# Optimization experiments

Hardware: AMD Instinct MI355X
Metric: run time of the kernel (lower is better)

The kernel has to match this reference:

```python
import jax, jax.numpy as jnp
import numpy as np

NEG_SLOPE = 0.2
LN_EPS = 1e-5


def setup_inputs() -> dict:
    key = jax.random.key(0)
    kx, kw, ks, kd = jax.random.split(key, 4)
    B, T, C, Fin, Fout = 32, 256, 64, 128, 128
    x = jax.random.normal(kx, (B, T, C, Fin), dtype=jnp.float32)
    W = jax.random.normal(kw, (Fin, Fout), dtype=jnp.float32) * (1.0 / np.sqrt(Fin))
    attn_src = jax.random.normal(ks, (Fout,), dtype=jnp.float32) * 0.1
    attn_dst = jax.random.normal(kd, (Fout,), dtype=jnp.float32) * 0.1
    gamma = jnp.ones((Fout,), dtype=jnp.float32)
    beta = jnp.zeros((Fout,), dtype=jnp.float32)
    return {"x": x, "W": W, "attn_src": attn_src, "attn_dst": attn_dst,
            "gamma": gamma, "beta": beta}


def reference(x, W, attn_src, attn_dst, gamma, beta):
    # h: (B,T,C,Fout)
    h = jnp.einsum('btci,io->btco', x, W)
    src = jnp.einsum('btcf,f->btc', h, attn_src)  # score of node as source
    dst = jnp.einsum('btcf,f->btc', h, attn_dst)  # score of node as dest
    # e[b,t,i,j] = src[b,t,i] + dst[b,t,j]
    e = src[..., :, None] + dst[..., None, :]
    e = jnp.where(e >= 0, e, NEG_SLOPE * e)  # leaky_relu
    alpha = jax.nn.softmax(e, axis=-1)       # softmax over neighbors j
    out = jnp.einsum('btij,btjf->btif', alpha, h)
    # LayerNorm over feature dim
    mu = jnp.mean(out, axis=-1, keepdims=True)
    var = jnp.var(out, axis=-1, keepdims=True)
    out = (out - mu) * jax.lax.rsqrt(var + LN_EPS) * gamma + beta
    return jax.nn.relu(out)
```

## Files before the change

### kernel.cpp

```cpp
#include <hip/hip_runtime.h>


typedef __attribute__((ext_vector_type(8))) short short8;
typedef __attribute__((ext_vector_type(4))) float f32x4;

constexpr int   NTILES    = 8192;
constexpr int   GRID      = 768;
constexpr float NEG_SLOPE = 0.2f;
constexpr float LN_EPS    = 1e-5f;

__device__ __forceinline__ unsigned short f2bf(float f) {
    unsigned int u = __builtin_bit_cast(unsigned int, f);
    return (unsigned short)((u + 0x7FFFu + ((u >> 16) & 1u)) >> 16);
}
__device__ __forceinline__ unsigned pack2(float lo, float hi) {
    return (unsigned)f2bf(lo) | ((unsigned)f2bf(hi) << 16);
}
__device__ __forceinline__ unsigned swz256(int row, int bytecol) {
    return (unsigned)(row * 256 + bytecol) ^ (unsigned)((row & 7) << 4);
}
__device__ __forceinline__ unsigned swz128(int row, int bytecol) {
    return (unsigned)(row * 128 + bytecol) ^ (unsigned)((row & 7) << 4);
}

#define LBAR() do { asm volatile("s_waitcnt lgkmcnt(0)"); __builtin_amdgcn_s_barrier(); } while (0)

__launch_bounds__(256, 3)
__global__ void gat_mfma7(const float* __restrict__ x,
                          const float* __restrict__ W,
                          const float* __restrict__ a_src,
                          const float* __restrict__ a_dst,
                          const float* __restrict__ gamma,
                          const float* __restrict__ beta,
                          float* __restrict__ out)
{
    __shared__ __align__(16) unsigned short sWt[128 * 128];
    __shared__ __align__(16) unsigned short sXH[64 * 128];
    __shared__ __align__(16) float s_src[64];
    __shared__ __align__(16) float s_dst[64];
    __shared__ __align__(16) float s_ws[128];
    __shared__ __align__(16) float s_wd[128];
    __shared__ __align__(16) float s_g[128];
    __shared__ __align__(16) float s_b[128];

    const int t    = threadIdx.x;
    const int lane = t & 63;
    const int w    = t >> 6;
    const int l15  = lane & 15;
    const int lg   = lane >> 4;

    if (t < 128) {
        const float4* W4  = reinterpret_cast<const float4*>(W) + t * 32;
        const float4* as4 = reinterpret_cast<const float4*>(a_src);
        const float4* ad4 = reinterpret_cast<const float4*>(a_dst);
        float ws = 0.f, wd = 0.f;
        for (int n4 = 0; n4 < 32; ++n4) {
            float4 wr = W4[n4], as = as4[n4], ad = ad4[n4];
            ws += wr.x*as.x + wr.y*as.y + wr.z*as.z + wr.w*as.w;
            wd += wr.x*ad.x + wr.y*ad.y + wr.z*ad.z + wr.w*ad.w;
        }
        s_ws[t] = ws; s_wd[t] = wd;
        s_g[t] = gamma[t]; s_b[t] = beta[t];
    }

    {
        const float4* W4 = reinterpret_cast<const float4*>(W);
        for (int c = 0; c < 16; ++c) {
            int idx4 = t + 256 * c;
            float4 v = W4[idx4];
            int k  = idx4 >> 5;
            int n0 = (idx4 & 31) << 2;
            *(unsigned short*)((char*)sWt + swz256(n0 + 0, k * 2)) = f2bf(v.x);
            *(unsigned short*)((char*)sWt + swz256(n0 + 1, k * 2)) = f2bf(v.y);
            *(unsigned short*)((char*)sWt + swz256(n0 + 2, k * 2)) = f2bf(v.z);
            *(unsigned short*)((char*)sWt + swz256(n0 + 3, k * 2)) = f2bf(v.w);
        }
    }
    __syncthreads();

    float wsr[8], wdr[8];
    {
        const int k0 = (t & 15) * 8;
        #pragma unroll
        for (int q = 0; q < 8; ++q) { wsr[q] = s_ws[k0 + q]; wdr[q] = s_wd[k0 + q]; }
    }

    float4 px[8];
    {
        const float4* x4 = reinterpret_cast<const float4*>(x + (size_t)blockIdx.x * 8192);
        #pragma unroll
        for (int c = 0; c < 4; ++c) {
            const int idx8 = t + 256 * c;
            px[2*c]   = x4[idx8 * 2];
            px[2*c+1] = x4[idx8 * 2 + 1];
        }
    }

    for (int tile = blockIdx.x; tile < NTILES; tile += GRID) {
        float* ob = out + (size_t)tile * 8192;

        #pragma unroll
        for (int c = 0; c < 4; ++c) {
            const float4 v0 = px[2*c], v1 = px[2*c+1];
            float ps = v0.x*wsr[0] + v0.y*wsr[1] + v0.z*wsr[2] + v0.w*wsr[3]
                     + v1.x*wsr[4] + v1.y*wsr[5] + v1.z*wsr[6] + v1.w*wsr[7];
            float pd = v0.x*wdr[0] + v0.y*wdr[1] + v0.z*wdr[2] + v0.w*wdr[3]
                     + v1.x*wdr[4] + v1.y*wdr[5] + v1.z*wdr[6] + v1.w*wdr[7];
            uint4 pk;
            pk.x = pack2(v0.x, v0.y); pk.y = pack2(v0.z, v0.w);
            pk.z = pack2(v1.x, v1.y); pk.w = pack2(v1.z, v1.w);
            const int m = (t >> 4) + 16 * c;
            *(uint4*)((char*)sXH + swz256(m, (t & 15) * 16)) = pk;
            #pragma unroll
            for (int msk = 1; msk < 16; msk <<= 1) {
                ps += __shfl_xor(ps, msk, 64);
                pd += __shfl_xor(pd, msk, 64);
            }
            if ((t & 15) == 0) { s_src[m] = ps; s_dst[m] = pd; }
        }

        if (tile + GRID < NTILES) {
            const float4* xn = reinterpret_cast<const float4*>(x + (size_t)(tile + GRID) * 8192);
            #pragma unroll
            for (int c = 0; c < 4; ++c) {
                const int idx8 = t + 256 * c;
                px[2*c]   = xn[idx8 * 2];
                px[2*c+1] = xn[idx8 * 2 + 1];
            }
        }
        LBAR();

        f32x4 acc[4][2];
        #pragma unroll
        for (int mi = 0; mi < 4; ++mi) {
            acc[mi][0] = f32x4{0.f,0.f,0.f,0.f};
            acc[mi][1] = f32x4{0.f,0.f,0.f,0.f};
        }
        #pragma unroll
        for (int kb = 0; kb < 4; ++kb) {
            const int kbyte = kb * 64 + lg * 16;
            short8 bfr0 = *(const short8*)((char*)sWt + swz256(32 * w +  0 + l15, kbyte));
            short8 bfr1 = *(const short8*)((char*)sWt + swz256(32 * w + 16 + l15, kbyte));
            #pragma unroll
            for (int mi = 0; mi < 4; ++mi) {
                short8 afr = *(const short8*)((char*)sXH + swz256(mi * 16 + l15, kbyte));
                acc[mi][0] = __builtin_amdgcn_mfma_f32_16x16x32_bf16(afr, bfr0, acc[mi][0], 0, 0, 0);
                acc[mi][1] = __builtin_amdgcn_mfma_f32_16x16x32_bf16(afr, bfr1, acc[mi][1], 0, 0, 0);
            }
        }

        short8 pa0, pa1;
        {
            const float srci = s_src[w * 16 + l15];
            const float4 dA0 = *(const float4*)&s_dst[lg * 8];
            const float4 dA1 = *(const float4*)&s_dst[lg * 8 + 4];
            const float4 dB0 = *(const float4*)&s_dst[32 + lg * 8];
            const float4 dB1 = *(const float4*)&s_dst[32 + lg * 8 + 4];
            float e[16] = { srci+dA0.x, srci+dA0.y, srci+dA0.z, srci+dA0.w,
                            srci+dA1.x, srci+dA1.y, srci+dA1.z, srci+dA1.w,
                            srci+dB0.x, srci+dB0.y, srci+dB0.z, srci+dB0.w,
                            srci+dB1.x, srci+dB1.y, srci+dB1.z, srci+dB1.w };
            float mx = -1e30f;
            #pragma unroll
            for (int q = 0; q < 16; ++q) {
                e[q] = (e[q] >= 0.f) ? e[q] : NEG_SLOPE * e[q];
                mx = fmaxf(mx, e[q]);
            }
            mx = fmaxf(mx, __shfl_xor(mx, 16, 64));
            mx = fmaxf(mx, __shfl_xor(mx, 32, 64));
            float sm = 0.f;
            #pragma unroll
            for (int q = 0; q < 16; ++q) { e[q] = __expf(e[q] - mx); sm += e[q]; }
            sm += __shfl_xor(sm, 16, 64);
            sm += __shfl_xor(sm, 32, 64);
            const float inv = 1.0f / sm;
            uint4 p0, p1;
            p0.x = pack2(e[0]*inv,  e[1]*inv);  p0.y = pack2(e[2]*inv,  e[3]*inv);
            p0.z = pack2(e[4]*inv,  e[5]*inv);  p0.w = pack2(e[6]*inv,  e[7]*inv);
            p1.x = pack2(e[8]*inv,  e[9]*inv);  p1.y = pack2(e[10]*inv, e[11]*inv);
            p1.z = pack2(e[12]*inv, e[13]*inv); p1.w = pack2(e[14]*inv, e[15]*inv);
            pa0 = __builtin_bit_cast(short8, p0);
            pa1 = __builtin_bit_cast(short8, p1);
        }
        LBAR();

        #pragma unroll
        for (int mi = 0; mi < 4; ++mi) {
            const int m0 = mi * 16 + lg * 4;
            #pragma unroll
            for (int nb = 0; nb < 2; ++nb) {
                const int n = 32 * w + nb * 16 + l15;
                uint2 pk;
                pk.x = pack2(acc[mi][nb][0], acc[mi][nb][1]);
                pk.y = pack2(acc[mi][nb][2], acc[mi][nb][3]);
                *(uint2*)((char*)sXH + swz128(n, m0 * 2)) = pk;
            }
        }
        LBAR();

        f32x4 o[8];
        #pragma unroll
        for (int mi = 0; mi < 8; ++mi) o[mi] = f32x4{0.f,0.f,0.f,0.f};
        #pragma unroll
        for (int kb = 0; kb < 2; ++kb) {
            const int jbyte = kb * 64 + lg * 16;
            const short8 bfr = (kb == 0) ? pa0 : pa1;
            #pragma unroll
            for (int mi = 0; mi < 8; ++mi) {
                short8 afr = *(const short8*)((char*)sXH + swz128(mi * 16 + l15, jbyte));
                o[mi] = __builtin_amdgcn_mfma_f32_16x16x32_bf16(afr, bfr, o[mi], 0, 0, 0);
            }
        }

        float sm1 = 0.f, sm2 = 0.f;
        #pragma unroll
        for (int mi = 0; mi < 8; ++mi) {
            #pragma unroll
            for (int r = 0; r < 4; ++r) { const float v = o[mi][r]; sm1 += v; sm2 += v * v; }
        }
        sm1 += __shfl_xor(sm1, 16, 64); sm2 += __shfl_xor(sm2, 16, 64);
        sm1 += __shfl_xor(sm1, 32, 64); sm2 += __shfl_xor(sm2, 32, 64);
        const float mu   = sm1 * (1.f / 128.f);
        const float var  = sm2 * (1.f / 128.f) - mu * mu;
        const float rstd = rsqrtf(var + LN_EPS);

        float* orow = ob + (w * 16 + l15) * 128;
        #pragma unroll
        for (int mi = 0; mi < 8; ++mi) {
            const int n0 = mi * 16 + lg * 4;
            const float4 gv = *(const float4*)&s_g[n0];
            const float4 bv = *(const float4*)&s_b[n0];
            float4 vo;
            vo.x = fmaxf((o[mi][0] - mu) * rstd * gv.x + bv.x, 0.f);
            vo.y = fmaxf((o[mi][1] - mu) * rstd * gv.y + bv.y, 0.f);
            vo.z = fmaxf((o[mi][2] - mu) * rstd * gv.z + bv.z, 0.f);
            vo.w = fmaxf((o[mi][3] - mu) * rstd * gv.w + bv.w, 0.f);
            *(float4*)(orow + n0) = vo;
        }
        LBAR();
    }
}

extern "C" void kernel_launch(void* const* d_in, const int* in_sizes, int n_in,
                              void* d_out, int out_size, void* d_ws, size_t ws_size,
                              hipStream_t stream) {
    const float* x   = (const float*)d_in[0];
    const float* W   = (const float*)d_in[1];
    const float* asv = (const float*)d_in[2];
    const float* adv = (const float*)d_in[3];
    const float* gm  = (const float*)d_in[4];
    const float* bt  = (const float*)d_in[5];
    float* out = (float*)d_out;

    hipLaunchKernelGGL(gat_mfma7, dim3(GRID), dim3(256), 0, stream,
                       x, W, asv, adv, gm, bt, out);
}
```

Baseline: 132.3 us.

## Double-buffer X staging and keep W fragments in registers

Moves the bf16 W operand out of shared memory into per-wave register fragments, which frees LDS for a second X/H buffer. Staging and score computation for the next tile now run one iteration ahead into the alternate buffer, and the global x prefetch goes two tiles ahead. The change removes one barrier per tile and the LDS reads of W, and adds sched_barrier fences around each barrier. In exchange it raises register pressure from 32 extra VGPRs of W fragments under a 3-blocks launch bound, and W is now read from global with strided scalar loads at startup.

Result: slower. 181.4 us (+37.1%).

```diff
diff --git a/kernel.cpp b/kernel.cpp
--- a/kernel.cpp
+++ b/kernel.cpp
@@ -23,21 +23,49 @@
     return (unsigned)(row * 128 + bytecol) ^ (unsigned)((row & 7) << 4);
 }
 
-#define LBAR() do { asm volatile("s_waitcnt lgkmcnt(0)"); __builtin_amdgcn_s_barrier(); } while (0)
+#define LBAR() do {                                              \
+    __builtin_amdgcn_sched_barrier(0);                           \
+    asm volatile("s_waitcnt lgkmcnt(0)" ::: "memory");           \
+    __builtin_amdgcn_s_barrier();                                \
+    __builtin_amdgcn_sched_barrier(0);                           \
+} while (0)
+
+#define STAGE_AND_SCORES(buf, psrc, pdst)                                     \
+    do {                                                                      \
+        _Pragma("unroll")                                                     \
+        for (int c = 0; c < 4; ++c) {                                         \
+            const float4 v0 = px[2*c], v1 = px[2*c+1];                        \
+            float ps = v0.x*wsr[0] + v0.y*wsr[1] + v0.z*wsr[2] + v0.w*wsr[3]  \
+                     + v1.x*wsr[4] + v1.y*wsr[5] + v1.z*wsr[6] + v1.w*wsr[7]; \
+            float pd = v0.x*wdr[0] + v0.y*wdr[1] + v0.z*wdr[2] + v0.w*wdr[3]  \
+                     + v1.x*wdr[4] + v1.y*wdr[5] + v1.z*wdr[6] + v1.w*wdr[7]; \
+            uint4 pk;                                                         \
+            pk.x = pack2(v0.x, v0.y); pk.y = pack2(v0.z, v0.w);               \
+            pk.z = pack2(v1.x, v1.y); pk.w = pack2(v1.z, v1.w);               \
+            const int m = (t >> 4) + 16 * c;                                  \
+            *(uint4*)((char*)(buf) + swz256(m, (t & 15) * 16)) = pk;          \
+            _Pragma("unroll")                                                 \
+            for (int msk = 1; msk < 16; msk <<= 1) {                          \
+                ps += __shfl_xor(ps, msk, 64);                                \
+                pd += __shfl_xor(pd, msk, 64);                                \
+            }                                                                 \
+            if ((t & 15) == 0) { (psrc)[m] = ps; (pdst)[m] = pd; }            \
+        }                                                                     \
+    } while (0)
 
 __launch_bounds__(256, 3)
-__global__ void gat_mfma7(const float* __restrict__ x,
-                          const float* __restrict__ W,
-                          const float* __restrict__ a_src,
-                          const float* __restrict__ a_dst,
-                          const float* __restrict__ gamma,
-                          const float* __restrict__ beta,
-                          float* __restrict__ out)
+__global__ void gat_mfma10(const float* __restrict__ x,
+                           const float* __restrict__ W,
+                           const float* __restrict__ a_src,
+                           const float* __restrict__ a_dst,
+                           const float* __restrict__ gamma,
+                           const float* __restrict__ beta,
+                           float* __restrict__ out)
 {
-    __shared__ __align__(16) unsigned short sWt[128 * 128];
-    __shared__ __align__(16) unsigned short sXH[64 * 128];
-    __shared__ __align__(16) float s_src[64];
-    __shared__ __align__(16) float s_dst[64];
+    __shared__ __align__(16) unsigned short sB0[64 * 128];
+    __shared__ __align__(16) unsigned short sB1[64 * 128];
+    __shared__ __align__(16) float s_src2[2][64];
+    __shared__ __align__(16) float s_dst2[2][64];
     __shared__ __align__(16) float s_ws[128];
     __shared__ __align__(16) float s_wd[128];
     __shared__ __align__(16) float s_g[128];
@@ -63,17 +91,20 @@
         s_g[t] = gamma[t]; s_b[t] = beta[t];
     }
 
-    {
-        const float4* W4 = reinterpret_cast<const float4*>(W);
-        for (int c = 0; c < 16; ++c) {
-            int idx4 = t + 256 * c;
-            float4 v = W4[idx4];
-            int k  = idx4 >> 5;
-            int n0 = (idx4 & 31) << 2;
-            *(unsigned short*)((char*)sWt + swz256(n0 + 0, k * 2)) = f2bf(v.x);
-            *(unsigned short*)((char*)sWt + swz256(n0 + 1, k * 2)) = f2bf(v.y);
-            *(unsigned short*)((char*)sWt + swz256(n0 + 2, k * 2)) = f2bf(v.z);
-            *(unsigned short*)((char*)sWt + swz256(n0 + 3, k * 2)) = f2bf(v.w);
+    short8 wfrag[2][4];
+    #pragma unroll
+    for (int nb = 0; nb < 2; ++nb) {
+        #pragma unroll
+        for (int kb = 0; kb < 4; ++kb) {
+            const int n = 32 * w + nb * 16 + l15;
+            float v[8];
+            #pragma unroll
+            for (int q = 0; q < 8; ++q)
+                v[q] = W[(kb * 32 + lg * 8 + q) * 128 + n];
+            uint4 pfr;
+            pfr.x = pack2(v[0], v[1]); pfr.y = pack2(v[2], v[3]);
+            pfr.z = pack2(v[4], v[5]); pfr.w = pack2(v[6], v[7]);
+            wfrag[nb][kb] = __builtin_bit_cast(short8, pfr);
         }
     }
     __syncthreads();
@@ -95,32 +126,29 @@
             px[2*c+1] = x4[idx8 * 2 + 1];
         }
     }
-
+    STAGE_AND_SCORES(sB0, s_src2[0], s_dst2[0]);
+    {
+        const float4* xn = reinterpret_cast<const float4*>(x + (size_t)(blockIdx.x + GRID) * 8192);
+        #pragma unroll
+        for (int c = 0; c < 4; ++c) {
+            const int idx8 = t + 256 * c;
+            px[2*c]   = xn[idx8 * 2];
+            px[2*c+1] = xn[idx8 * 2 + 1];
+        }
+    }
+    __syncthreads();
+
+    int p = 0;
     for (int tile = blockIdx.x; tile < NTILES; tile += GRID) {
         float* ob = out + (size_t)tile * 8192;
-
-        #pragma unroll
-        for (int c = 0; c < 4; ++c) {
-            const float4 v0 = px[2*c], v1 = px[2*c+1];
-            float ps = v0.x*wsr[0] + v0.y*wsr[1] + v0.z*wsr[2] + v0.w*wsr[3]
-                     + v1.x*wsr[4] + v1.y*wsr[5] + v1.z*wsr[6] + v1.w*wsr[7];
-            float pd = v0.x*wdr[0] + v0.y*wdr[1] + v0.z*wdr[2] + v0.w*wdr[3]
-                     + v1.x*wdr[4] + v1.y*wdr[5] + v1.z*wdr[6] + v1.w*wdr[7];
-            uint4 pk;
-            pk.x = pack2(v0.x, v0.y); pk.y = pack2(v0.z, v0.w);
-            pk.z = pack2(v1.x, v1.y); pk.w = pack2(v1.z, v1.w);
-            const int m = (t >> 4) + 16 * c;
-            *(uint4*)((char*)sXH + swz256(m, (t & 15) * 16)) = pk;
-            #pragma unroll
-            for (int msk = 1; msk < 16; msk <<= 1) {
-                ps += __shfl_xor(ps, msk, 64);
-                pd += __shfl_xor(pd, msk, 64);
-            }
-            if ((t & 15) == 0) { s_src[m] = ps; s_dst[m] = pd; }
-        }
+        unsigned short* cur = p ? sB1 : sB0;
+        unsigned short* nxt = p ? sB0 : sB1;
 
         if (tile + GRID < NTILES) {
-            const float4* xn = reinterpret_cast<const float4*>(x + (size_t)(tile + GRID) * 8192);
+            STAGE_AND_SCORES(nxt, s_src2[p ^ 1], s_dst2[p ^ 1]);
+        }
+        if (tile + 2 * GRID < NTILES) {
+            const float4* xn = reinterpret_cast<const float4*>(x + (size_t)(tile + 2 * GRID) * 8192);
             #pragma unroll
             for (int c = 0; c < 4; ++c) {
                 const int idx8 = t + 256 * c;
@@ -128,7 +156,6 @@
                 px[2*c+1] = xn[idx8 * 2 + 1];
             }
         }
-        LBAR();
 
         f32x4 acc[4][2];
         #pragma unroll
@@ -139,18 +166,33 @@
         #pragma unroll
         for (int kb = 0; kb < 4; ++kb) {
             const int kbyte = kb * 64 + lg * 16;
-            short8 bfr0 = *(const short8*)((char*)sWt + swz256(32 * w +  0 + l15, kbyte));
-            short8 bfr1 = *(const short8*)((char*)sWt + swz256(32 * w + 16 + l15, kbyte));
             #pragma unroll
             for (int mi = 0; mi < 4; ++mi) {
-                short8 afr = *(const short8*)((char*)sXH + swz256(mi * 16 + l15, kbyte));
-                acc[mi][0] = __builtin_amdgcn_mfma_f32_16x16x32_bf16(afr, bfr0, acc[mi][0], 0, 0, 0);
-                acc[mi][1] = __builtin_amdgcn_mfma_f32_16x16x32_bf16(afr, bfr1, acc[mi][1], 0, 0, 0);
-            }
-        }
+                short8 afr = *(const short8*)((char*)cur + swz256(mi * 16 + l15, kbyte));
+                acc[mi][0] = __builtin_amdgcn_mfma_f32_16x16x32_bf16(afr, wfrag[0][kb], acc[mi][0], 0, 0, 0);
+                acc[mi][1] = __builtin_amdgcn_mfma_f32_16x16x32_bf16(afr, wfrag[1][kb], acc[mi][1], 0, 0, 0);
+            }
+        }
+        LBAR();
+
+        #pragma unroll
+        for (int mi = 0; mi < 4; ++mi) {
+            const int m0 = mi * 16 + lg * 4;
+            #pragma unroll
+            for (int nb = 0; nb < 2; ++nb) {
+                const int n = 32 * w + nb * 16 + l15;
+                uint2 pk;
+                pk.x = pack2(acc[mi][nb][0], acc[mi][nb][1]);
+                pk.y = pack2(acc[mi][nb][2], acc[mi][nb][3]);
+                *(uint2*)((char*)cur + swz128(n, m0 * 2)) = pk;
+            }
+        }
+        LBAR();
 
         short8 pa0, pa1;
         {
+            const float* s_src = s_src2[p];
+            const float* s_dst = s_dst2[p];
             const float srci = s_src[w * 16 + l15];
             const float4 dA0 = *(const float4*)&s_dst[lg * 8];
             const float4 dA1 = *(const float4*)&s_dst[lg * 8 + 4];
@@ -182,21 +224,6 @@
             pa0 = __builtin_bit_cast(short8, p0);
             pa1 = __builtin_bit_cast(short8, p1);
         }
-        LBAR();
-
-        #pragma unroll
-        for (int mi = 0; mi < 4; ++mi) {
-            const int m0 = mi * 16 + lg * 4;
-            #pragma unroll
-            for (int nb = 0; nb < 2; ++nb) {
-                const int n = 32 * w + nb * 16 + l15;
-                uint2 pk;
-                pk.x = pack2(acc[mi][nb][0], acc[mi][nb][1]);
-                pk.y = pack2(acc[mi][nb][2], acc[mi][nb][3]);
-                *(uint2*)((char*)sXH + swz128(n, m0 * 2)) = pk;
-            }
-        }
-        LBAR();
 
         f32x4 o[8];
         #pragma unroll
@@ -207,7 +234,7 @@
             const short8 bfr = (kb == 0) ? pa0 : pa1;
             #pragma unroll
             for (int mi = 0; mi < 8; ++mi) {
-                short8 afr = *(const short8*)((char*)sXH + swz128(mi * 16 + l15, jbyte));
+                short8 afr = *(const short8*)((char*)cur + swz128(mi * 16 + l15, jbyte));
                 o[mi] = __builtin_amdgcn_mfma_f32_16x16x32_bf16(afr, bfr, o[mi], 0, 0, 0);
             }
         }
@@ -238,6 +265,7 @@
             *(float4*)(orow + n0) = vo;
         }
         LBAR();
+        p ^= 1;
     }
 }
 
@@ -252,6 +280,6 @@
     const float* bt  = (const float*)d_in[5];
     float* out = (float*)d_out;
 
-    hipLaunchKernelGGL(gat_mfma7, dim3(GRID), dim3(256), 0, stream,
+    hipLaunchKernelGGL(gat_mfma10, dim3(GRID), dim3(256), 0, stream,
                        x, W, asv, adv, gm, bt, out);
 }
```
